# Kernel tuning notes

Measured on AMD Instinct MI355X. Metric: run time of the kernel, lower is better.

The kernel has to match this reference:

```python
import jax, jax.numpy as jnp
import numpy as np

NUM_HEADS = 8


def _layernorm(x, w, b, eps=1e-5):
    # normalize over last axis (channels)
    mu = jnp.mean(x, axis=-1, keepdims=True)
    var = jnp.var(x, axis=-1, keepdims=True)
    return (x - mu) * jax.lax.rsqrt(var + eps) * w + b


def setup_inputs() -> dict:
    key = jax.random.key(0)
    ks = jax.random.split(key, 5)
    B, C, H, W = 8, 512, 32, 32
    x = jax.random.normal(ks[0], (B, C, H, W), dtype=jnp.float32)
    ln_w = jnp.ones((C,), dtype=jnp.float32)
    ln_b = jnp.zeros((C,), dtype=jnp.float32)
    qkv_w = jax.random.normal(ks[1], (3 * C, C), dtype=jnp.float32) * (1.0 / np.sqrt(C))
    qkv_b = jax.random.normal(ks[2], (3 * C,), dtype=jnp.float32) * 0.02
    proj_w = jax.random.normal(ks[3], (C, C), dtype=jnp.float32) * (1.0 / np.sqrt(C))
    proj_b = jax.random.normal(ks[4], (C,), dtype=jnp.float32) * 0.02
    return {"x": x, "ln_w": ln_w, "ln_b": ln_b, "qkv_w": qkv_w,
            "qkv_b": qkv_b, "proj_w": proj_w, "proj_b": proj_b}


def reference(x, ln_w, ln_b, qkv_w, qkv_b, proj_w, proj_b):
    B, C, H, W = x.shape
    nh = NUM_HEADS
    hd = C // nh
    HW = H * W
    residual = x
    # LayerNorm over channels: (B,C,H,W) -> (B,H,W,C)
    xn = _layernorm(x.transpose(0, 2, 3, 1), ln_w, ln_b)  # (B,H,W,C)
    # 1x1 conv == per-pixel linear: (B,H,W,3C)
    qkv = jnp.einsum('bhwc,oc->bhwo', xn, qkv_w) + qkv_b
    # match torch reshape (B,3,nh,hd,HW).permute(1,0,2,4,3)
    qkv = qkv.reshape(B, HW, 3, nh, hd).transpose(2, 0, 3, 1, 4)  # (3,B,nh,HW,hd)
    q, k, v = qkv[0], qkv[1], qkv[2]
    scale = 1.0 / jnp.sqrt(jnp.asarray(hd, dtype=x.dtype))
    attn = jnp.einsum('bnqd,bnkd->bnqk', q, k) * scale  # (B,nh,HW,HW)
    attn = jax.nn.softmax(attn, axis=-1)
    out = jnp.einsum('bnqk,bnkd->bnqd', attn, v)  # (B,nh,HW,hd)
    out = out.transpose(0, 2, 1, 3).reshape(B, H, W, C)
    out = jnp.einsum('bhwc,oc->bhwo', out, proj_w) + proj_b
    return out.transpose(0, 3, 1, 2) + residual
```

## Files before the change

### kernel.cpp

```cpp
#include <hip/hip_runtime.h>

typedef __bf16 bf16;
typedef __bf16 bf16x8 __attribute__((ext_vector_type(8)));
typedef float f32x4 __attribute__((ext_vector_type(4)));

#define MFMA16(a, b, c) __builtin_amdgcn_mfma_f32_16x16x32_bf16(a, b, c, 0, 0, 0)

#define QSCALE 0.1803368801111137f

static __device__ __forceinline__ unsigned int pack2(float a, float b) {
  unsigned short s0 = __builtin_bit_cast(unsigned short, (bf16)a);
  unsigned short s1 = __builtin_bit_cast(unsigned short, (bf16)b);
  return (unsigned int)s0 | ((unsigned int)s1 << 16);
}

static __device__ __forceinline__ void gl16(const bf16* g, bf16* l) {
  __builtin_amdgcn_global_load_lds(
      (const __attribute__((address_space(1))) unsigned int*)g,
      (__attribute__((address_space(3))) unsigned int*)l, 16, 0, 0);
}

__global__ __launch_bounds__(256) void convert_w(const float* __restrict__ qkvw,
                                                 const float* __restrict__ projw,
                                                 bf16* __restrict__ wc) {
  int c4 = blockIdx.x * 256 + threadIdx.x;
  const float* src = (c4 < 196608) ? (qkvw + (size_t)c4 * 4)
                                   : (projw + (size_t)(c4 - 196608) * 4);
  float4 v = *(const float4*)src;
  uint2 o;
  o.x = pack2(v.x, v.y);
  o.y = pack2(v.z, v.w);
  *(uint2*)&wc[(size_t)c4 * 4] = o;
}

__global__ __launch_bounds__(256) void ln_kernel(const float* __restrict__ x,
                                                 const float* __restrict__ lnw,
                                                 const float* __restrict__ lnb,
                                                 bf16* __restrict__ xn) {
  __shared__ float tile[512 * 17];
  __shared__ float wsh[512];
  __shared__ float bsh[512];
  const int t = threadIdx.x;
  const int b = blockIdx.x >> 6;
  const int p0 = (blockIdx.x & 63) * 16;
  for (int i = t; i < 512; i += 256) {
    wsh[i] = lnw[i];
    bsh[i] = lnb[i];
  }
  const float* xb = x + (size_t)b * 524288 + p0;
#pragma unroll
  for (int i = 0; i < 8; ++i) {
    int chunk = t + 256 * i;
    int c = chunk >> 2, px4 = (chunk & 3) * 4;
    float4 v = *(const float4*)&xb[(size_t)c * 1024 + px4];
    tile[c * 17 + px4 + 0] = v.x;
    tile[c * 17 + px4 + 1] = v.y;
    tile[c * 17 + px4 + 2] = v.z;
    tile[c * 17 + px4 + 3] = v.w;
  }
  __syncthreads();
  const int pix = t >> 4, j = t & 15;
  float sum = 0.f, sq = 0.f;
#pragma unroll
  for (int i = 0; i < 32; ++i) {
    int c = i * 16 + j;
    float v = tile[c * 17 + pix];
    sum += v;
    sq += v * v;
  }
#pragma unroll
  for (int m = 1; m <= 8; m <<= 1) {
    sum += __shfl_xor(sum, m);
    sq += __shfl_xor(sq, m);
  }
  float mu = sum * (1.f / 512.f);
  float var = sq * (1.f / 512.f) - mu * mu;
  float rstd = rsqrtf(var + 1e-5f);
  unsigned int* orow =
      (unsigned int*)(xn + ((size_t)(b * 1024 + p0 + pix)) * 512);
#pragma unroll
  for (int i = 0; i < 16; ++i) {
    int dw = i * 16 + j;
    int c0 = 2 * dw, c1 = 2 * dw + 1;
    float v0 = (tile[c0 * 17 + pix] - mu) * rstd * wsh[c0] + bsh[c0];
    float v1 = (tile[c1 * 17 + pix] - mu) * rstd * wsh[c1] + bsh[c1];
    orow[dw] = pack2(v0, v1);
  }
}

__global__ __launch_bounds__(256, 3) void gemm_qkv(
    const bf16* __restrict__ A, const bf16* __restrict__ Bm,
    const float* __restrict__ bias, bf16* __restrict__ oq,
    bf16* __restrict__ okk, bf16* __restrict__ ov) {
  __shared__ bf16 smem[16384];
  bf16* ash = smem;
  bf16* bsh = smem + 8192;
  const int t = threadIdx.x;
  const int lane = t & 63, w = t >> 6;
  const int quad = lane >> 4, r16 = lane & 15;
  const int wm = w >> 1, wn = w & 1;
  const int pid = blockIdx.x;
  const int panel = pid / 96, within = pid % 96;
  const int m0 = (panel * 8 + (within & 7)) * 128;
  const int n0 = (within >> 3) * 128;
  int soff[4];
  int sr[4];
#pragma unroll
  for (int j = 0; j < 4; ++j) {
    int c = (w * 4 + j) * 64 + lane;
    int r = c >> 3, cc = c & 7;
    sr[j] = r;
    soff[j] = (cc ^ (r & 7)) * 8;
  }
  f32x4 acc[4][4] = {};
  for (int k0 = 0; k0 < 512; k0 += 64) {
#pragma unroll
    for (int j = 0; j < 4; ++j) {
      gl16(&A[(size_t)(m0 + sr[j]) * 512 + k0 + soff[j]],
           &ash[(w * 4 + j) * 512]);
      gl16(&Bm[(size_t)(n0 + sr[j]) * 512 + k0 + soff[j]],
           &bsh[(w * 4 + j) * 512]);
    }
    __syncthreads();
#pragma unroll
    for (int kc = 0; kc < 2; ++kc) {
      bf16x8 af[4], bfr[4];
#pragma unroll
      for (int i = 0; i < 4; ++i) {
        int row = wm * 64 + i * 16 + r16;
        af[i] = *(const bf16x8*)&ash[row * 64 +
                                     ((kc * 4 + quad) ^ (r16 & 7)) * 8];
      }
#pragma unroll
      for (int i = 0; i < 4; ++i) {
        int row = wn * 64 + i * 16 + r16;
        bfr[i] = *(const bf16x8*)&bsh[row * 64 +
                                      ((kc * 4 + quad) ^ (r16 & 7)) * 8];
      }
#pragma unroll
      for (int tm = 0; tm < 4; ++tm)
#pragma unroll
        for (int tn = 0; tn < 4; ++tn)
          acc[tm][tn] = MFMA16(af[tm], bfr[tn], acc[tm][tn]);
    }
    __syncthreads();
  }
  if (n0 < 1024) {
#pragma unroll
    for (int tm = 0; tm < 4; ++tm) {
#pragma unroll
      for (int tn = 0; tn < 4; ++tn) {
        int n = n0 + wn * 64 + tn * 16 + r16;
        float bn = bias[n];
        int comp = n >> 9, h = (n >> 6) & 7, d = n & 63;
#pragma unroll
        for (int r = 0; r < 4; ++r) {
          int m = m0 + wm * 64 + tm * 16 + quad * 4 + r;
          float v = acc[tm][tn][r] + bn;
          int b = m >> 10, p = m & 1023;
          size_t base = ((size_t)(b * 8 + h)) * 65536;
          if (comp == 0)
            oq[base + (size_t)p * 64 + d] = (bf16)(v * QSCALE);
          else
            okk[base + (size_t)p * 64 + d] = (bf16)v;
        }
      }
    }
  } else {
    bf16* tb = &smem[w * 4096];
#pragma unroll
    for (int tn = 0; tn < 4; ++tn) {
      int n = n0 + wn * 64 + tn * 16 + r16;
      float bn = bias[n];
      int row = tn * 16 + r16;
#pragma unroll
      for (int tm = 0; tm < 4; ++tm) {
        f32x4 a = acc[tm][tn];
        uint2 pk;
        pk.x = pack2(a[0] + bn, a[1] + bn);
        pk.y = pack2(a[2] + bn, a[3] + bn);
        int g = (tm * 2 + (quad >> 1)) ^ (row & 7);
        *(uint2*)&tb[row * 64 + g * 8 + (quad & 1) * 4] = pk;
      }
    }
    const int h = ((n0 - 1024) >> 6) + wn;
    const int mw = m0 + wm * 64;
    const int b = mw >> 10;
    bf16* vbase = ov + ((size_t)(b * 8 + h)) * 65536 + (mw & 1023);
#pragma unroll
    for (int pass = 0; pass < 8; ++pass) {
      int row = pass * 8 + (lane >> 3);
      int g = (lane & 7) ^ (row & 7);
      uint4 vd = *(uint4*)&tb[row * 64 + g * 8];
      *(uint4*)&vbase[(size_t)row * 1024 + (lane & 7) * 8] = vd;
    }
  }
}

__global__ __launch_bounds__(256, 4) void gemm_proj(
    const bf16* __restrict__ Wm, const bf16* __restrict__ A,
    const float* __restrict__ bias, const float* __restrict__ resid,
    float* __restrict__ op) {
  __shared__ bf16 ash[2][64 * 64];
  __shared__ bf16 bsh[2][64 * 64];
  const int t = threadIdx.x;
  const int lane = t & 63, w = t >> 6;
  const int quad = lane >> 4, r16 = lane & 15;
  const int wm = w >> 1, wn = w & 1;
  const int m0 = blockIdx.x * 64, n0 = blockIdx.y * 64;
  int soff[2], sr[2];
#pragma unroll
  for (int j = 0; j < 2; ++j) {
    int c = (w * 2 + j) * 64 + lane;
    int r = c >> 3, cc = c & 7;
    sr[j] = r;
    soff[j] = (cc ^ (r & 7)) * 8;
  }
  f32x4 acc[2][2] = {};
#pragma unroll
  for (int j = 0; j < 2; ++j) {
    gl16(&Wm[(size_t)(m0 + sr[j]) * 512 + soff[j]], &ash[0][(w * 2 + j) * 512]);
    gl16(&A[(size_t)(n0 + sr[j]) * 512 + soff[j]], &bsh[0][(w * 2 + j) * 512]);
  }
  __syncthreads();
  for (int it = 0; it < 8; ++it) {
    const int cur = it & 1, nxt = cur ^ 1;
    if (it < 7) {
      int k1 = (it + 1) * 64;
#pragma unroll
      for (int j = 0; j < 2; ++j) {
        gl16(&Wm[(size_t)(m0 + sr[j]) * 512 + k1 + soff[j]],
             &ash[nxt][(w * 2 + j) * 512]);
        gl16(&A[(size_t)(n0 + sr[j]) * 512 + k1 + soff[j]],
             &bsh[nxt][(w * 2 + j) * 512]);
      }
    }
#pragma unroll
    for (int kc = 0; kc < 2; ++kc) {
      bf16x8 af[2], bfr[2];
#pragma unroll
      for (int i = 0; i < 2; ++i) {
        int row = wm * 32 + i * 16 + r16;
        af[i] = *(const bf16x8*)&ash[cur][row * 64 +
                                          ((kc * 4 + quad) ^ (r16 & 7)) * 8];
      }
#pragma unroll
      for (int i = 0; i < 2; ++i) {
        int row = wn * 32 + i * 16 + r16;
        bfr[i] = *(const bf16x8*)&bsh[cur][row * 64 +
                                           ((kc * 4 + quad) ^ (r16 & 7)) * 8];
      }
#pragma unroll
      for (int tm = 0; tm < 2; ++tm)
#pragma unroll
        for (int tn = 0; tn < 2; ++tn)
          acc[tm][tn] = MFMA16(af[tm], bfr[tn], acc[tm][tn]);
    }
    __syncthreads();
  }
#pragma unroll
  for (int tm = 0; tm < 2; ++tm) {
#pragma unroll
    for (int tn = 0; tn < 2; ++tn) {
      int n = n0 + wn * 32 + tn * 16 + r16;
      int b = n >> 10, p = n & 1023;
#pragma unroll
      for (int r = 0; r < 4; ++r) {
        int m = m0 + wm * 32 + tm * 16 + quad * 4 + r;
        size_t idx = ((size_t)(b * 512 + m)) * 1024 + p;
        op[idx] = acc[tm][tn][r] + bias[m] + resid[idx];
      }
    }
  }
}

__global__ __launch_bounds__(256, 4) void attn_kernel(
    const bf16* __restrict__ q, const bf16* __restrict__ k,
    const bf16* __restrict__ vT, bf16* __restrict__ o) {
  __shared__ bf16 kt[2][64 * 64];
  __shared__ bf16 vt[2][64 * 64];
  __shared__ bf16 psh[4][16 * 40];
  const int t = threadIdx.x;
  const int lane = t & 63, w = t >> 6;
  const int quad = lane >> 4, r16 = lane & 15;
  const int bh = blockIdx.x;
  const int qt0 = blockIdx.y * 64;
  const bf16* qb = q + (size_t)bh * 65536;
  const bf16* kb = k + (size_t)bh * 65536;
  const bf16* vb = vT + (size_t)bh * 65536;
  const int qrow = qt0 + w * 16 + r16;
  bf16x8 qf0 = *(const bf16x8*)&qb[(size_t)qrow * 64 + quad * 8];
  bf16x8 qf1 = *(const bf16x8*)&qb[(size_t)qrow * 64 + 32 + quad * 8];
  int offk[2], offv[2];
#pragma unroll
  for (int j = 0; j < 2; ++j) {
    int c = (w * 2 + j) * 64 + lane;
    int r = c >> 3, cc = c & 7;
    int sw = (cc ^ (r & 7)) * 8;
    offk[j] = r * 64 + sw;
    offv[j] = r * 1024 + sw;
  }
  f32x4 rsum = {};
  f32x4 oacc[4] = {};
  bf16* pw = psh[w];
  const int swz = r16 & 7;
#pragma unroll
  for (int j = 0; j < 2; ++j) {
    gl16(&kb[offk[j]], &kt[0][(w * 2 + j) * 512]);
    gl16(&vb[offv[j]], &vt[0][(w * 2 + j) * 512]);
  }
  __syncthreads();
  for (int it = 0; it < 16; ++it) {
    const int cur = it & 1, nxt = cur ^ 1;
    if (it < 15) {
      int kv1 = (it + 1) * 64;
#pragma unroll
      for (int j = 0; j < 2; ++j) {
        gl16(&kb[(size_t)kv1 * 64 + offk[j]], &kt[nxt][(w * 2 + j) * 512]);
        gl16(&vb[(size_t)kv1 + offv[j]], &vt[nxt][(w * 2 + j) * 512]);
      }
    }
    const bf16* ktc = kt[cur];
    const bf16* vtc = vt[cur];
    f32x4 s[4];
#pragma unroll
    for (int tn = 0; tn < 4; ++tn) {
      const bf16* kr = &ktc[(tn * 16 + r16) * 64];
      bf16x8 kf0 = *(const bf16x8*)&kr[(quad ^ swz) * 8];
      bf16x8 kf1 = *(const bf16x8*)&kr[((4 + quad) ^ swz) * 8];
      f32x4 z = {};
      z = MFMA16(qf0, kf0, z);
      z = MFMA16(qf1, kf1, z);
      s[tn] = z;
    }
#pragma unroll
    for (int tn = 0; tn < 4; ++tn)
#pragma unroll
      for (int r = 0; r < 4; ++r) {
        float p = __builtin_exp2f(s[tn][r]);
        s[tn][r] = p;
        rsum[r] += p;
      }
#pragma unroll
    for (int kc = 0; kc < 2; ++kc) {
#pragma unroll
      for (int tt = 0; tt < 2; ++tt)
#pragma unroll
        for (int r = 0; r < 4; ++r)
          pw[(quad * 4 + r) * 40 + tt * 16 + r16] = (bf16)s[kc * 2 + tt][r];
      bf16x8 pf = *(const bf16x8*)&pw[r16 * 40 + quad * 8];
#pragma unroll
      for (int tn = 0; tn < 4; ++tn) {
        const bf16* vr = &vtc[(tn * 16 + r16) * 64];
        bf16x8 vf = *(const bf16x8*)&vr[((kc * 4 + quad) ^ swz) * 8];
        oacc[tn] = MFMA16(pf, vf, oacc[tn]);
      }
    }
    __syncthreads();
  }
#pragma unroll
  for (int msk = 1; msk <= 8; msk <<= 1)
#pragma unroll
    for (int r = 0; r < 4; ++r) rsum[r] += __shfl_xor(rsum[r], msk);
  float inv[4];
#pragma unroll
  for (int r = 0; r < 4; ++r) inv[r] = 1.f / rsum[r];
  const int b = bh >> 3, h = bh & 7;
#pragma unroll
  for (int tn = 0; tn < 4; ++tn)
#pragma unroll
    for (int r = 0; r < 4; ++r) {
      int p = qt0 + w * 16 + quad * 4 + r;
      o[((size_t)(b * 1024 + p)) * 512 + h * 64 + tn * 16 + r16] =
          (bf16)(oacc[tn][r] * inv[r]);
    }
}

extern "C" void kernel_launch(void* const* d_in, const int* in_sizes, int n_in,
                              void* d_out, int out_size, void* d_ws,
                              size_t ws_size, hipStream_t stream) {
  (void)in_sizes;
  (void)n_in;
  (void)out_size;
  (void)ws_size;
  const float* x = (const float*)d_in[0];
  const float* lnw = (const float*)d_in[1];
  const float* lnb = (const float*)d_in[2];
  const float* qkvw = (const float*)d_in[3];
  const float* qkvb = (const float*)d_in[4];
  const float* projw = (const float*)d_in[5];
  const float* projb = (const float*)d_in[6];
  float* out = (float*)d_out;

  const size_t NELEM = 4194304;
  bf16* wc = (bf16*)d_ws;
  bf16* xn = wc + 1048576;
  bf16* qws = xn + NELEM;
  bf16* kws = qws + NELEM;
  bf16* vws = kws + NELEM;
  bf16* aws = xn;

  convert_w<<<dim3(1024), dim3(256), 0, stream>>>(qkvw, projw, wc);
  ln_kernel<<<dim3(512), dim3(256), 0, stream>>>(x, lnw, lnb, xn);
  gemm_qkv<<<dim3(768), dim3(256), 0, stream>>>(xn, wc, qkvb, qws, kws, vws);
  attn_kernel<<<dim3(64, 16), dim3(256), 0, stream>>>(qws, kws, vws, aws);
  gemm_proj<<<dim3(8, 128), dim3(256), 0, stream>>>(wc + 786432, aws, projb, x,
                                                    out);
}
```

Baseline: 160.1 us.

## Rewrite attention with 32x32 MFMA computing S^T to keep P in registers

The attention kernel now uses 32x32x16 bf16 MFMAs and computes the transposed score tile (K·Q^T), so each lane's exp'd probabilities can be packed directly into the B-operand layout for the PV MFMA. This removes the per-wave LDS round trip for P and the 16-lane shuffle reduction of row sums. Each block now handles 128 query rows (half the grid), and launch bounds drop to 2 blocks/CU to allow more registers. The V-tile store swizzle in gemm_qkv changes to match the new read pattern. Fewer blocks and higher register use may reduce occupancy and latency hiding.

```diff
diff --git a/kernel.cpp b/kernel.cpp
--- a/kernel.cpp
+++ b/kernel.cpp
@@ -3,8 +3,10 @@
 typedef __bf16 bf16;
 typedef __bf16 bf16x8 __attribute__((ext_vector_type(8)));
 typedef float f32x4 __attribute__((ext_vector_type(4)));
+typedef float f32x16 __attribute__((ext_vector_type(16)));
 
 #define MFMA16(a, b, c) __builtin_amdgcn_mfma_f32_16x16x32_bf16(a, b, c, 0, 0, 0)
+#define MFMA32(a, b, c) __builtin_amdgcn_mfma_f32_32x32x16_bf16(a, b, c, 0, 0, 0)
 
 #define QSCALE 0.1803368801111137f
 
@@ -179,8 +181,8 @@
         uint2 pk;
         pk.x = pack2(a[0] + bn, a[1] + bn);
         pk.y = pack2(a[2] + bn, a[3] + bn);
-        int g = (tm * 2 + (quad >> 1)) ^ (row & 7);
-        *(uint2*)&tb[row * 64 + g * 8 + (quad & 1) * 4] = pk;
+        int g = (tm * 2 + (quad & 1)) ^ (row & 7);
+        *(uint2*)&tb[row * 64 + g * 8 + (quad >> 1) * 4] = pk;
       }
     }
     const int h = ((n0 - 1024) >> 6) + wn;
@@ -274,23 +276,24 @@
   }
 }
 
-__global__ __launch_bounds__(256, 4) void attn_kernel(
+__global__ __launch_bounds__(256, 2) void attn_kernel(
     const bf16* __restrict__ q, const bf16* __restrict__ k,
     const bf16* __restrict__ vT, bf16* __restrict__ o) {
   __shared__ bf16 kt[2][64 * 64];
   __shared__ bf16 vt[2][64 * 64];
-  __shared__ bf16 psh[4][16 * 40];
   const int t = threadIdx.x;
   const int lane = t & 63, w = t >> 6;
-  const int quad = lane >> 4, r16 = lane & 15;
+  const int l31 = lane & 31, hi = lane >> 5;
   const int bh = blockIdx.x;
-  const int qt0 = blockIdx.y * 64;
+  const int qt0 = blockIdx.y * 128;
   const bf16* qb = q + (size_t)bh * 65536;
   const bf16* kb = k + (size_t)bh * 65536;
   const bf16* vb = vT + (size_t)bh * 65536;
-  const int qrow = qt0 + w * 16 + r16;
-  bf16x8 qf0 = *(const bf16x8*)&qb[(size_t)qrow * 64 + quad * 8];
-  bf16x8 qf1 = *(const bf16x8*)&qb[(size_t)qrow * 64 + 32 + quad * 8];
+  const int qrow = qt0 + w * 32 + l31;
+  bf16x8 qf[4];
+#pragma unroll
+  for (int ks = 0; ks < 4; ++ks)
+    qf[ks] = *(const bf16x8*)&qb[(size_t)qrow * 64 + ks * 16 + hi * 8];
   int offk[2], offv[2];
 #pragma unroll
   for (int j = 0; j < 2; ++j) {
@@ -300,10 +303,9 @@
     offk[j] = r * 64 + sw;
     offv[j] = r * 1024 + sw;
   }
-  f32x4 rsum = {};
-  f32x4 oacc[4] = {};
-  bf16* pw = psh[w];
-  const int swz = r16 & 7;
+  f32x16 oacc[2] = {};
+  float rsum = 0.f;
+  const int swz = l31 & 7;
 #pragma unroll
   for (int j = 0; j < 2; ++j) {
     gl16(&kb[offk[j]], &kt[0][(w * 2 + j) * 512]);
@@ -322,58 +324,55 @@
     }
     const bf16* ktc = kt[cur];
     const bf16* vtc = vt[cur];
-    f32x4 s[4];
-#pragma unroll
-    for (int tn = 0; tn < 4; ++tn) {
-      const bf16* kr = &ktc[(tn * 16 + r16) * 64];
-      bf16x8 kf0 = *(const bf16x8*)&kr[(quad ^ swz) * 8];
-      bf16x8 kf1 = *(const bf16x8*)&kr[((4 + quad) ^ swz) * 8];
-      f32x4 z = {};
-      z = MFMA16(qf0, kf0, z);
-      z = MFMA16(qf1, kf1, z);
-      s[tn] = z;
-    }
-#pragma unroll
-    for (int tn = 0; tn < 4; ++tn)
-#pragma unroll
-      for (int r = 0; r < 4; ++r) {
-        float p = __builtin_exp2f(s[tn][r]);
-        s[tn][r] = p;
-        rsum[r] += p;
-      }
-#pragma unroll
-    for (int kc = 0; kc < 2; ++kc) {
-#pragma unroll
-      for (int tt = 0; tt < 2; ++tt)
-#pragma unroll
-        for (int r = 0; r < 4; ++r)
-          pw[(quad * 4 + r) * 40 + tt * 16 + r16] = (bf16)s[kc * 2 + tt][r];
-      bf16x8 pf = *(const bf16x8*)&pw[r16 * 40 + quad * 8];
-#pragma unroll
-      for (int tn = 0; tn < 4; ++tn) {
-        const bf16* vr = &vtc[(tn * 16 + r16) * 64];
-        bf16x8 vf = *(const bf16x8*)&vr[((kc * 4 + quad) ^ swz) * 8];
-        oacc[tn] = MFMA16(pf, vf, oacc[tn]);
+    f32x16 sT[2] = {};
+#pragma unroll
+    for (int T = 0; T < 2; ++T) {
+      const bf16* kr = &ktc[(T * 32 + l31) * 64];
+#pragma unroll
+      for (int ks = 0; ks < 4; ++ks) {
+        bf16x8 kf = *(const bf16x8*)&kr[((ks * 2 + hi) ^ swz) * 8];
+        sT[T] = MFMA32(kf, qf[ks], sT[T]);
+      }
+    }
+#pragma unroll
+    for (int T = 0; T < 2; ++T)
+#pragma unroll
+      for (int r = 0; r < 16; ++r) {
+        float p = __builtin_exp2f(sT[T][r]);
+        sT[T][r] = p;
+        rsum += p;
+      }
+#pragma unroll
+    for (int c4 = 0; c4 < 4; ++c4) {
+      const int T = c4 >> 1, b0 = (c4 & 1) * 8;
+      uint4 pui;
+      pui.x = pack2(sT[T][b0 + 0], sT[T][b0 + 1]);
+      pui.y = pack2(sT[T][b0 + 2], sT[T][b0 + 3]);
+      pui.z = pack2(sT[T][b0 + 4], sT[T][b0 + 5]);
+      pui.w = pack2(sT[T][b0 + 6], sT[T][b0 + 7]);
+      bf16x8 pf = __builtin_bit_cast(bf16x8, pui);
+#pragma unroll
+      for (int mf = 0; mf < 2; ++mf) {
+        const bf16* vr = &vtc[(mf * 32 + l31) * 64];
+        bf16x8 vf = *(const bf16x8*)&vr[((c4 * 2 + hi) ^ swz) * 8];
+        oacc[mf] = MFMA32(pf, vf, oacc[mf]);
       }
     }
     __syncthreads();
   }
-#pragma unroll
-  for (int msk = 1; msk <= 8; msk <<= 1)
-#pragma unroll
-    for (int r = 0; r < 4; ++r) rsum[r] += __shfl_xor(rsum[r], msk);
-  float inv[4];
-#pragma unroll
-  for (int r = 0; r < 4; ++r) inv[r] = 1.f / rsum[r];
+  rsum += __shfl_xor(rsum, 32);
+  float inv = 1.f / rsum;
   const int b = bh >> 3, h = bh & 7;
 #pragma unroll
-  for (int tn = 0; tn < 4; ++tn)
-#pragma unroll
-    for (int r = 0; r < 4; ++r) {
-      int p = qt0 + w * 16 + quad * 4 + r;
-      o[((size_t)(b * 1024 + p)) * 512 + h * 64 + tn * 16 + r16] =
-          (bf16)(oacc[tn][r] * inv[r]);
-    }
+  for (int r = 0; r < 16; ++r) {
+    const int ql = (r & 3) + 8 * (r >> 2) + 4 * hi;
+    float invq = __shfl(inv, ql);
+    const int p = qt0 + w * 32 + ql;
+    const size_t base = ((size_t)(b * 1024 + p)) * 512 + h * 64;
+#pragma unroll
+    for (int mf = 0; mf < 2; ++mf)
+      o[base + mf * 32 + l31] = (bf16)(oacc[mf][r] * invq);
+  }
 }
 
 extern "C" void kernel_launch(void* const* d_in, const int* in_sizes, int n_in,
@@ -403,7 +402,7 @@
   convert_w<<<dim3(1024), dim3(256), 0, stream>>>(qkvw, projw, wc);
   ln_kernel<<<dim3(512), dim3(256), 0, stream>>>(x, lnw, lnb, xn);
   gemm_qkv<<<dim3(768), dim3(256), 0, stream>>>(xn, wc, qkvb, qws, kws, vws);
-  attn_kernel<<<dim3(64, 16), dim3(256), 0, stream>>>(qws, kws, vws, aws);
+  attn_kernel<<<dim3(64, 8), dim3(256), 0, stream>>>(qws, kws, vws, aws);
   gemm_proj<<<dim3(8, 128), dim3(256), 0, stream>>>(wc + 786432, aws, projb, x,
                                                     out);
 }
```

Result: faster. 153.3 us (-4.3%).
